# Optimization experiments

Hardware: AMD Instinct MI355X
Metric: run time of the kernel (lower is better)

Reference implementation:

```python
import jax, jax.numpy as jnp
import numpy as np

EPS = 1e-4

@jax.custom_vjp
def binarize(x):
    # BinaryConnectDeterministic: sign with sign(0)=+1
    return jnp.where(x >= 0, 1.0, -1.0).astype(x.dtype)

def _bin_fwd(x):
    return binarize(x), x

def _bin_bwd(x, g):
    # straight-through estimator, clipped to |x| <= 1
    return (g * (jnp.abs(x) <= 1).astype(g.dtype),)

binarize.defvjp(_bin_fwd, _bin_bwd)

def ap2(x):
    # approximate power-of-2: sign(x) * 2^round(log2|x|); grad is 0 a.e. (round/sign)
    a = jnp.maximum(jnp.abs(x), 1e-38)
    return jnp.sign(x) * jnp.exp2(jnp.round(jnp.log2(a)))

def shift_bn(x, gamma, beta, axes):
    # shift-based batch norm (BNN paper): var approximated via centered*AP2(centered),
    # inverse std and gamma replaced by their AP2 approximations. Training-mode batch stats.
    mean = jnp.mean(x, axis=axes, keepdims=True)
    c = x - mean
    var = jnp.mean(c * ap2(c), axis=axes, keepdims=True)
    xhat = c * ap2(1.0 / jnp.sqrt(var + EPS))
    shape = [1] * x.ndim
    shape[1] = x.shape[1]
    return ap2(gamma.reshape(shape)) * xhat + beta.reshape(shape)

def conv_bin(x, w, b):
    y = jax.lax.conv_general_dilated(x, binarize(w), (1, 1), [(1, 1), (1, 1)],
                                     dimension_numbers=('NCHW', 'OIHW', 'NCHW'))
    return y + b[None, :, None, None]

def maxpool3s2(x):
    return jax.lax.reduce_window(x, -jnp.inf, jax.lax.max,
                                 (1, 1, 3, 3), (1, 1, 2, 2), 'VALID')


def setup_inputs() -> dict:
    key = jax.random.key(0)
    ks = jax.random.split(key, 8)
    B, NU = 2048, 2048
    inp = {
        'x': jax.random.normal(ks[0], (B, 784), jnp.float32),
        'conv1_w': jax.random.normal(ks[1], (32, 1, 3, 3), jnp.float32) * 0.1,
        'conv1_b': jnp.zeros((32,), jnp.float32),
        'g1': jnp.ones((32,), jnp.float32), 'b1': jnp.zeros((32,), jnp.float32),
        'conv2_w': jax.random.normal(ks[2], (64, 32, 3, 3), jnp.float32) * 0.1,
        'conv2_b': jnp.zeros((64,), jnp.float32),
        'g2': jnp.ones((64,), jnp.float32), 'b2': jnp.zeros((64,), jnp.float32),
        'lin3_w': jax.random.normal(ks[3], (NU, 10816), jnp.float32) * 0.02,
        'lin3_b': jnp.zeros((NU,), jnp.float32),
        'g3': jnp.ones((NU,), jnp.float32), 'b3': jnp.zeros((NU,), jnp.float32),
        'lin4_w': jax.random.normal(ks[4], (10, NU), jnp.float32) * 0.02,
        'lin4_b': jnp.zeros((10,), jnp.float32),
    }
    return inp


def reference(x, conv1_w, conv1_b, g1, b1, conv2_w, conv2_b, g2, b2,
              lin3_w, lin3_b, g3, b3, lin4_w, lin4_b):
    h = x.reshape(-1, 1, 28, 28)
    h = jax.nn.relu(conv_bin(h, conv1_w, conv1_b))
    h = shift_bn(h, g1, b1, axes=(0, 2, 3))
    h = binarize(h)
    h = jax.nn.relu(conv_bin(h, conv2_w, conv2_b))
    h = maxpool3s2(h)                       # [B,64,13,13]
    h = shift_bn(h, g2, b2, axes=(0, 2, 3))
    h = binarize(h)
    h = h.reshape(h.shape[0], -1)           # [B,10816]
    h = jax.nn.relu(h @ binarize(lin3_w).T + lin3_b)
    h = shift_bn(h, g3, b3, axes=(0,))
    h = binarize(h)
    return h @ binarize(lin4_w).T + lin4_b  # [B,10] (no norm4/logsoftmax in forward)
```

## Files before the change

kernel.cpp:

```cpp
#include <hip/hip_runtime.h>

#define BB 2048
#define IMG 784
#define HWD 28
#define C1 32
#define C2 64
#define PP 169
#define PD 13
#define F3 10816
#define N3 2048
#define K4W 32
#define NOUT 10
#define CONV 27
#define PADW 30
#define OCCHUNK 8
#define IMGC 29
#define SCRP 740

typedef unsigned long long u64;
typedef int v4i __attribute__((ext_vector_type(4)));
typedef int v16i __attribute__((ext_vector_type(16)));

#define GLOAD16(gp, lp) __builtin_amdgcn_global_load_lds( \
    (__attribute__((address_space(1))) void*)(gp),        \
    (__attribute__((address_space(3))) void*)(lp), 16, 0, 0)

__device__ __forceinline__ float ap2mag(float c) {
    unsigned int a = __float_as_uint(c) & 0x7fffffffu;
    unsigned int e = (a >> 23) + ((a & 0x7fffffu) > 0x3504f3u);
    return __uint_as_float(e << 23);
}
__device__ __forceinline__ float ap2sgn(float g) {
    unsigned int u = __float_as_uint(g);
    unsigned int a = u & 0x7fffffffu;
    if (a == 0) return 0.f;
    unsigned int e = (a >> 23) + ((a & 0x7fffffu) > 0x3504f3u);
    return __uint_as_float((u & 0x80000000u) | (e << 23));
}

__global__ __launch_bounds__(256) void stage0(const float* __restrict__ x,
                                              const float* __restrict__ w1, const float* __restrict__ cb1,
                                              float* __restrict__ part1, float* __restrict__ w1b,
                                              const float* __restrict__ w2, char* __restrict__ w2i8,
                                              const float* __restrict__ w3, char* __restrict__ wp3i,
                                              const float* __restrict__ w4, u64* __restrict__ wp4) {
    __shared__ float xs[30 * PADW];
    __shared__ float red[4 * C1];
    int n = blockIdx.x, tid = threadIdx.x;
    int lane = tid & 63, wv = tid >> 6;
    {
        int idx = n * 256 + tid;
        int nthr = gridDim.x * 256;
        int total = (N3 * F3) / 4;
        for (int t = idx; t < total; t += nthr) {
            float4 wv4 = *(const float4*)(w3 + (size_t)t * 4);
            unsigned int w = (wv4.x >= 0.f ? 0x01u : 0xffu)
                           | (wv4.y >= 0.f ? 0x01u : 0xffu) << 8
                           | (wv4.z >= 0.f ? 0x01u : 0xffu) << 16
                           | (wv4.w >= 0.f ? 0x01u : 0xffu) << 24;
            *(unsigned int*)(wp3i + (size_t)t * 4) = w;
        }
    }
    if (n == 0) {
        for (int i = tid; i < C1 * 9; i += 256) w1b[i] = (w1[i] >= 0.f) ? 1.f : -1.f;
    } else if (n == 1) {
        for (int i = tid; i < 2 * 9 * 64 * 16; i += 256) {
            int hf = i / 9216;
            int r = i - hf * 9216;
            int t = r >> 10;
            int l = (r >> 4) & 63;
            int j = i & 15;
            int oc = hf * 32 + (l & 31);
            int ic = ((l >> 5) << 4) + j;
            w2i8[i] = (w2[oc * 288 + ic * 9 + t] >= 0.f) ? (char)1 : (char)(-1);
        }
    } else if (n == 2) {
        for (int w = wv; w < NOUT * K4W; w += 4) {
            int o = w / K4W, j = w % K4W;
            float wvl = w4[o * N3 + j * 64 + lane];
            u64 mask = __ballot(wvl >= 0.f);
            if (lane == 0) wp4[w] = mask;
        }
    }
    for (int i = tid; i < 30 * PADW; i += 256) {
        int r = i / PADW - 1, c = i % PADW - 1;
        float v = 0.f;
        if (r >= 0 && r < HWD && c >= 0 && c < HWD) v = x[n * IMG + r * HWD + c];
        xs[i] = v;
    }
    __syncthreads();
    bool act = tid < 196;
    int r = tid / 7, c0 = (tid % 7) * 4;
    float win[18];
#pragma unroll
    for (int k = 0; k < 18; k++) win[k] = 0.f;
    if (act) {
#pragma unroll
        for (int ry = 0; ry < 3; ry++)
#pragma unroll
            for (int cx = 0; cx < 6; cx++)
                win[ry * 6 + cx] = xs[(r + ry) * PADW + c0 + cx];
    }
#pragma unroll
    for (int ch = 0; ch < C1; ch++) {
        float a = 0.f;
        if (act) {
            float k0 = (w1[ch * 9 + 0] >= 0.f) ? 1.f : -1.f, k1 = (w1[ch * 9 + 1] >= 0.f) ? 1.f : -1.f;
            float k2 = (w1[ch * 9 + 2] >= 0.f) ? 1.f : -1.f, k3 = (w1[ch * 9 + 3] >= 0.f) ? 1.f : -1.f;
            float k4 = (w1[ch * 9 + 4] >= 0.f) ? 1.f : -1.f, k5 = (w1[ch * 9 + 5] >= 0.f) ? 1.f : -1.f;
            float k6 = (w1[ch * 9 + 6] >= 0.f) ? 1.f : -1.f, k7 = (w1[ch * 9 + 7] >= 0.f) ? 1.f : -1.f;
            float k8 = (w1[ch * 9 + 8] >= 0.f) ? 1.f : -1.f;
            float b = cb1[ch];
#pragma unroll
            for (int px = 0; px < 4; px++) {
                float s = win[px] * k0 + win[px + 1] * k1 + win[px + 2] * k2
                        + win[6 + px] * k3 + win[7 + px] * k4 + win[8 + px] * k5
                        + win[12 + px] * k6 + win[13 + px] * k7 + win[14 + px] * k8;
                a += fmaxf(s + b, 0.f);
            }
        }
        for (int off = 32; off; off >>= 1) a += __shfl_down(a, off);
        if (lane == 0) red[wv * C1 + ch] = a;
    }
    __syncthreads();
    if (tid < C1) part1[n * C1 + tid] = red[tid] + red[C1 + tid] + red[2 * C1 + tid] + red[3 * C1 + tid];
}

__global__ __launch_bounds__(256) void conv1_var(const float* __restrict__ x,
                            const float* __restrict__ w1b,
                            const float* __restrict__ cb1, const float* __restrict__ mean1,
                            float* __restrict__ part) {
    __shared__ float xs[30 * PADW];
    __shared__ float red[4 * C1];
    int n = blockIdx.x, tid = threadIdx.x;
    for (int i = tid; i < 30 * PADW; i += 256) {
        int r = i / PADW - 1, c = i % PADW - 1;
        float v = 0.f;
        if (r >= 0 && r < HWD && c >= 0 && c < HWD) v = x[n * IMG + r * HWD + c];
        xs[i] = v;
    }
    __syncthreads();
    bool act = tid < 196;
    int r = tid / 7, c0 = (tid % 7) * 4;
    float win[18];
#pragma unroll
    for (int k = 0; k < 18; k++) win[k] = 0.f;
    if (act) {
#pragma unroll
        for (int ry = 0; ry < 3; ry++)
#pragma unroll
            for (int cx = 0; cx < 6; cx++)
                win[ry * 6 + cx] = xs[(r + ry) * PADW + c0 + cx];
    }
    int lane = tid & 63, wv = tid >> 6;
#pragma unroll
    for (int ch = 0; ch < C1; ch++) {
        float a = 0.f;
        if (act) {
            float k0 = w1b[ch * 9 + 0], k1 = w1b[ch * 9 + 1], k2 = w1b[ch * 9 + 2];
            float k3 = w1b[ch * 9 + 3], k4 = w1b[ch * 9 + 4], k5 = w1b[ch * 9 + 5];
            float k6 = w1b[ch * 9 + 6], k7 = w1b[ch * 9 + 7], k8 = w1b[ch * 9 + 8];
            float b = cb1[ch], m = mean1[ch];
#pragma unroll
            for (int px = 0; px < 4; px++) {
                float s = win[px] * k0 + win[px + 1] * k1 + win[px + 2] * k2
                        + win[6 + px] * k3 + win[7 + px] * k4 + win[8 + px] * k5
                        + win[12 + px] * k6 + win[13 + px] * k7 + win[14 + px] * k8;
                float v = fmaxf(s + b, 0.f);
                float c = v - m;
                a += fabsf(c) * ap2mag(c);
            }
        }
        for (int off = 32; off; off >>= 1) a += __shfl_down(a, off);
        if (lane == 0) red[wv * C1 + ch] = a;
    }
    __syncthreads();
    if (tid < C1) part[n * C1 + tid] = red[tid] + red[C1 + tid] + red[2 * C1 + tid] + red[3 * C1 + tid];
}

__global__ __launch_bounds__(256) void conv1_pack(const float* __restrict__ x,
                           const float* __restrict__ w1b,
                           const float* __restrict__ cb1, const float* __restrict__ mean1,
                           const float* __restrict__ scale1, const float* __restrict__ beta1,
                           unsigned int* __restrict__ s1p) {
    __shared__ float xs[30 * PADW];
    int n = blockIdx.x, tid = threadIdx.x;
    for (int i = tid; i < 30 * PADW; i += 256) {
        int r = i / PADW - 1, c = i % PADW - 1;
        float v = 0.f;
        if (r >= 0 && r < HWD && c >= 0 && c < HWD) v = x[n * IMG + r * HWD + c];
        xs[i] = v;
    }
    __syncthreads();
    if (tid >= 196) return;
    int r = tid / 7, c0 = (tid % 7) * 4;
    float win[18];
#pragma unroll
    for (int ry = 0; ry < 3; ry++)
#pragma unroll
        for (int cx = 0; cx < 6; cx++)
            win[ry * 6 + cx] = xs[(r + ry) * PADW + c0 + cx];
    unsigned int bits0 = 0, bits1 = 0, bits2 = 0, bits3 = 0;
#pragma unroll
    for (int ch = 0; ch < C1; ch++) {
        float k0 = w1b[ch * 9 + 0], k1 = w1b[ch * 9 + 1], k2 = w1b[ch * 9 + 2];
        float k3 = w1b[ch * 9 + 3], k4 = w1b[ch * 9 + 4], k5 = w1b[ch * 9 + 5];
        float k6 = w1b[ch * 9 + 6], k7 = w1b[ch * 9 + 7], k8 = w1b[ch * 9 + 8];
        float b = cb1[ch], m = mean1[ch], sc = scale1[ch], bt = beta1[ch];
#pragma unroll
        for (int px = 0; px < 4; px++) {
            float s = win[px] * k0 + win[px + 1] * k1 + win[px + 2] * k2
                    + win[6 + px] * k3 + win[7 + px] * k4 + win[8 + px] * k5
                    + win[12 + px] * k6 + win[13 + px] * k7 + win[14 + px] * k8;
            float v = fmaxf(s + b, 0.f);
            float val = sc * (v - m) + bt;
            unsigned int bit = (val >= 0.f ? 1u : 0u) << ch;
            if (px == 0) bits0 |= bit;
            else if (px == 1) bits1 |= bit;
            else if (px == 2) bits2 |= bit;
            else bits3 |= bit;
        }
    }
    uint4 w4v = make_uint4(bits0, bits1, bits2, bits3);
    *reinterpret_cast<uint4*>(&s1p[n * IMG + r * HWD + c0]) = w4v;
}

__global__ __launch_bounds__(256) void conv2pool(const unsigned int* __restrict__ s1p,
                                                 const char* __restrict__ w2i8,
                                                 const float* __restrict__ cb2,
                                                 short* __restrict__ p2i,
                                                 float* __restrict__ part2) {
    __shared__ char img[IMGC * IMGC * 32];
    __shared__ short scr[32 * SCRP];
    __shared__ float psum[OCCHUNK * PP];
    __shared__ float pm[C2];
    int n = blockIdx.x, tid = threadIdx.x;
    int lane = tid & 63, wv = tid >> 6;
    for (int i = tid; i < IMGC * IMGC; i += 256) {
        int r = i / IMGC, c = i - r * IMGC;
        unsigned int w = 0u;
        if (r >= 1 && c >= 1) w = s1p[n * IMG + (r - 1) * HWD + (c - 1)];
        unsigned int d[8];
        if (r == 0 || c == 0) {
#pragma unroll
            for (int e = 0; e < 8; e++) d[e] = 0u;
        } else {
#pragma unroll
            for (int e = 0; e < 8; e++) {
                unsigned int nib = (w >> (4 * e)) & 0xFu;
                unsigned int t = (nib & 1u) | ((nib & 2u) << 7) | ((nib & 4u) << 14) | ((nib & 8u) << 21);
                d[e] = 0xFFFFFFFFu - t * 0xFEu;
            }
        }
        *(uint4*)&img[i * 32] = make_uint4(d[0], d[1], d[2], d[3]);
        *(uint4*)&img[i * 32 + 16] = make_uint4(d[4], d[5], d[6], d[7]);
    }
    __syncthreads();
    int hh = lane >> 5;
    int l31 = lane & 31;
    for (int hf = 0; hf < 2; hf++) {
        v4i bf[9];
#pragma unroll
        for (int t = 0; t < 9; t++)
            bf[t] = *(const v4i*)(w2i8 + (hf * 9 + t) * 1024 + lane * 16);
#pragma unroll
        for (int j = 0; j < 3; j++) {
            int mtA = wv + 8 * j, mtB = mtA + 4;
            int pA = mtA * 32 + l31; if (pA > 728) pA = 728;
            int pB = mtB * 32 + l31; if (pB > 728) pB = 728;
            int yA = pA / 27, xA = pA - yA * 27;
            int yB = pB / 27, xB = pB - yB * 27;
            int aA = (yA * IMGC + xA) * 32 + hh * 16;
            int aB = (yB * IMGC + xB) * 32 + hh * 16;
            v16i accA = {0,0,0,0,0,0,0,0,0,0,0,0,0,0,0,0};
            v16i accB = {0,0,0,0,0,0,0,0,0,0,0,0,0,0,0,0};
#pragma unroll
            for (int ky = 0; ky < 3; ky++)
#pragma unroll
                for (int kx = 0; kx < 3; kx++) {
                    v4i fA = *(const v4i*)&img[aA + (ky * IMGC + kx) * 32];
                    v4i fB = *(const v4i*)&img[aB + (ky * IMGC + kx) * 32];
                    accA = __builtin_amdgcn_mfma_i32_32x32x32_i8(fA, bf[ky * 3 + kx], accA, 0, 0, 0);
                    accB = __builtin_amdgcn_mfma_i32_32x32x32_i8(fB, bf[ky * 3 + kx], accB, 0, 0, 0);
                }
            short* sr = &scr[l31 * SCRP];
#pragma unroll
            for (int g = 0; g < 4; g++) {
                short4 sA;
                sA.x = (short)accA[4 * g + 0]; sA.y = (short)accA[4 * g + 1];
                sA.z = (short)accA[4 * g + 2]; sA.w = (short)accA[4 * g + 3];
                *(short4*)&sr[mtA * 32 + g * 8 + 4 * hh] = sA;
            }
            if (mtB < 23) {
#pragma unroll
                for (int g = 0; g < 4; g++) {
                    short4 sB;
                    sB.x = (short)accB[4 * g + 0]; sB.y = (short)accB[4 * g + 1];
                    sB.z = (short)accB[4 * g + 2]; sB.w = (short)accB[4 * g + 3];
                    *(short4*)&sr[mtB * 32 + g * 8 + 4 * hh] = sB;
                }
            }
        }
        __syncthreads();
        for (int base = 0; base < 32; base += OCCHUNK) {
            for (int q = tid; q < OCCHUNK * PP; q += 256) {
                int ol = q / PP, pix = q - ol * PP;
                int py = pix / PD, px = pix - py * PD;
                const short* rr = &scr[(base + ol) * SCRP + (2 * py) * CONV + 2 * px];
                int m0 = max(max((int)rr[0], (int)rr[1]), (int)rr[2]);
                int m1 = max(max((int)rr[CONV], (int)rr[CONV + 1]), (int)rr[CONV + 2]);
                int m2 = max(max((int)rr[2 * CONV], (int)rr[2 * CONV + 1]), (int)rr[2 * CONV + 2]);
                int val = max(max(m0, m1), m2);
                int oc = hf * 32 + base + ol;
                p2i[n * F3 + oc * PP + pix] = (short)val;
                psum[q] = fmaxf((float)val + cb2[oc], 0.f);
            }
            __syncthreads();
            for (int ol = wv; ol < OCCHUNK; ol += 4) {
                float a = 0.f;
                for (int pp = lane; pp < PP; pp += 64) a += psum[ol * PP + pp];
                for (int off = 32; off; off >>= 1) a += __shfl_down(a, off);
                if (lane == 0) pm[hf * 32 + base + ol] = a;
            }
            __syncthreads();
        }
    }
    if (tid < C2) part2[n * C2 + tid] = pm[tid];
}

__global__ __launch_bounds__(256) void p2_var(const short* __restrict__ p2i,
                         const float* __restrict__ cb2,
                         const float* __restrict__ mean2, float* __restrict__ part) {
    int n = blockIdx.x, tid = threadIdx.x, lane = tid & 63, wv = tid >> 6;
    const short* rowb = p2i + (size_t)n * F3;
    __shared__ float red[C2];
#pragma unroll
    for (int i = 0; i < 16; i++) {
        int ch = wv * 16 + i;
        const short* row = rowb + ch * PP;
        float b = cb2[ch];
        float m = mean2[ch];
        float a = 0.f;
        for (int p = lane; p < PP; p += 64) {
            float v = fmaxf((float)row[p] + b, 0.f);
            float c = v - m;
            a += fabsf(c) * ap2mag(c);
        }
        for (int off = 32; off; off >>= 1) a += __shfl_down(a, off);
        if (lane == 0) red[ch] = a;
    }
    __syncthreads();
    if (tid < C2) part[n * C2 + tid] = red[tid];
}

__global__ __launch_bounds__(256) void reduce_stats(const float* __restrict__ part, int nch, int nblk,
                             const float* __restrict__ g, float* __restrict__ outv,
                             int mode, double count) {
    int ch = blockIdx.x, tid = threadIdx.x;
    double a = 0.0;
    for (int i = tid; i < nblk; i += 256) a += (double)part[(size_t)i * nch + ch];
    __shared__ double red[4];
    for (int off = 32; off; off >>= 1) a += __shfl_down(a, off);
    int lane = tid & 63, wv = tid >> 6;
    if (lane == 0) red[wv] = a;
    __syncthreads();
    if (tid == 0) {
        double s = red[0] + red[1] + red[2] + red[3];
        if (mode == 0) {
            outv[ch] = (float)(s / count);
        } else {
            float var = (float)(s / count);
            float inv = 1.0f / sqrtf(var + 1e-4f);
            outv[ch] = ap2sgn(g[ch]) * ap2mag(inv);
        }
    }
}

__global__ __launch_bounds__(256) void p2_packi8(const short* __restrict__ p2i, const float* __restrict__ cb2,
                        const float* __restrict__ mean2, const float* __restrict__ scale2,
                        const float* __restrict__ beta2, char* __restrict__ hp3i) {
    int idx = blockIdx.x * 256 + threadIdx.x;
    int nthr = gridDim.x * 256;
    int total = (BB * F3) / 4;
    for (int t = idx; t < total; t += nthr) {
        int base = t * 4;
        int f0 = base % F3;
        unsigned int w = 0;
#pragma unroll
        for (int e = 0; e < 4; e++) {
            int f = f0 + e;
            int oc = f / PP;
            float v = fmaxf((float)p2i[base + e] + cb2[oc], 0.f);
            float val = scale2[oc] * (v - mean2[oc]) + beta2[oc];
            w |= (val >= 0.f ? 0x01u : 0xffu) << (8 * e);
        }
        *(unsigned int*)(hp3i + base) = w;
    }
}

__global__ __launch_bounds__(512) void lin3_mfma(const char* __restrict__ hp3i,
                                                 const char* __restrict__ wp3i,
                                                 const float* __restrict__ b3l,
                                                 float* __restrict__ h3,
                                                 float* __restrict__ h3T,
                                                 float* __restrict__ part3) {
    __shared__ v4i aL[3][1024];
    __shared__ v4i bL[3][1024];
    __shared__ float csr[8][32];
    int tid = threadIdx.x;
    int lane = tid & 63, wv = tid >> 6;
    int wr = wv >> 2, wc = wv & 3;
    int m0 = blockIdx.y * 128, n0 = blockIdx.x * 128;
    int loff = (lane & 15) * F3 + (lane >> 4) * 16;
    const char* gA = hp3i + (size_t)(m0 + wv * 16) * F3 + loff;
    const char* gB = wp3i + (size_t)(n0 + wv * 16) * F3 + loff;
    v4i acc[4][2];
#pragma unroll
    for (int i = 0; i < 4; i++)
#pragma unroll
        for (int j = 0; j < 2; j++) acc[i][j] = (v4i){0, 0, 0, 0};

    auto stage = [&](int c) {
        int b = c % 3;
        const char* pA = gA + (size_t)c * 128;
        const char* pB = gB + (size_t)c * 128;
        char* dA = (char*)&aL[b][0] + wv * 1024;
        char* dB = (char*)&bL[b][0] + wv * 1024;
        GLOAD16(pA,      dA);
        GLOAD16(pA + 64, dA + 8192);
        GLOAD16(pB,      dB);
        GLOAD16(pB + 64, dB + 8192);
    };
    auto compute = [&](int c, int nks) {
        int b = c % 3;
        for (int ks = 0; ks < nks; ++ks) {
            v4i af[4], bf[2];
#pragma unroll
            for (int i = 0; i < 4; i++) af[i] = aL[b][ks * 512 + (wr * 4 + i) * 64 + lane];
#pragma unroll
            for (int j = 0; j < 2; j++) bf[j] = bL[b][ks * 512 + (wc * 2 + j) * 64 + lane];
            __builtin_amdgcn_s_setprio(1);
#pragma unroll
            for (int i = 0; i < 4; i++)
#pragma unroll
                for (int j = 0; j < 2; j++)
                    acc[i][j] = __builtin_amdgcn_mfma_i32_16x16x64_i8(af[i], bf[j], acc[i][j], 0, 0, 0);
            __builtin_amdgcn_s_setprio(0);
        }
    };

    stage(0); stage(1);
    asm volatile("s_waitcnt vmcnt(4)" ::: "memory");
    __builtin_amdgcn_s_barrier();
    __builtin_amdgcn_sched_barrier(0);
    for (int c = 0; c < 83; ++c) {
        stage(c + 2);
        compute(c, 2);
        asm volatile("s_waitcnt vmcnt(4)" ::: "memory");
        __builtin_amdgcn_s_barrier();
        __builtin_amdgcn_sched_barrier(0);
    }
    compute(83, 2);
    asm volatile("s_waitcnt vmcnt(0)" ::: "memory");
    __builtin_amdgcn_s_barrier();
    __builtin_amdgcn_sched_barrier(0);
    compute(84, 1);

    int q = lane >> 4, m16 = lane & 15;
    float cs[2] = {0.f, 0.f};
#pragma unroll
    for (int j = 0; j < 2; j++) {
        int col = n0 + wc * 32 + j * 16 + m16;
        float bias = b3l[col];
#pragma unroll
        for (int i = 0; i < 4; i++) {
            int rowb = m0 + wr * 64 + i * 16 + q * 4;
            float4 t4;
#pragma unroll
            for (int rg = 0; rg < 4; rg++) {
                float v = fmaxf((float)acc[i][j][rg] + bias, 0.f);
                h3[(size_t)(rowb + rg) * N3 + col] = v;
                ((float*)&t4)[rg] = v;
                cs[j] += v;
            }
            *(float4*)&h3T[(size_t)col * BB + rowb] = t4;
        }
    }
#pragma unroll
    for (int j = 0; j < 2; j++) {
        cs[j] += __shfl_xor(cs[j], 16);
        cs[j] += __shfl_xor(cs[j], 32);
        if (lane < 16) csr[wv][j * 16 + m16] = cs[j];
    }
    __syncthreads();
    if (tid < 128) {
        int wcg = tid >> 5, cc = tid & 31;
        part3[(size_t)blockIdx.y * N3 + n0 + tid] = csr[wcg][cc] + csr[4 + wcg][cc];
    }
}

__global__ __launch_bounds__(256) void h3_finish(const float* __restrict__ h3T,
                                                 const float* __restrict__ part3,
                                                 const float* __restrict__ g3,
                                                 float* __restrict__ mean3, float* __restrict__ scale3) {
    int nn = blockIdx.x, tid = threadIdx.x;
    __shared__ float msh;
    __shared__ double redd[4];
    if (tid < 64) {
        float a = (tid < 16) ? part3[(size_t)tid * N3 + nn] : 0.f;
        for (int off = 8; off; off >>= 1) a += __shfl_down(a, off);
        if (tid == 0) { float m = a / (float)BB; mean3[nn] = m; msh = m; }
    }
    __syncthreads();
    float m = msh;
    float acc = 0.f;
#pragma unroll
    for (int q = 0; q < 8; q++) {
        float v = h3T[(size_t)nn * BB + q * 256 + tid];
        float c = v - m;
        acc += fabsf(c) * ap2mag(c);
    }
    double a = (double)acc;
    for (int off = 32; off; off >>= 1) a += __shfl_down(a, off);
    int lane = tid & 63, wv = tid >> 6;
    if (lane == 0) redd[wv] = a;
    __syncthreads();
    if (tid == 0) {
        float var = (float)((redd[0] + redd[1] + redd[2] + redd[3]) / (double)BB);
        float inv = 1.0f / sqrtf(var + 1e-4f);
        scale3[nn] = ap2sgn(g3[nn]) * ap2mag(inv);
    }
}

__global__ __launch_bounds__(256) void h4_out(const float* __restrict__ h3,
                                              const float* __restrict__ mean3, const float* __restrict__ scale3,
                                              const float* __restrict__ bt3,
                                              const u64* __restrict__ wp4, const float* __restrict__ b4,
                                              float* __restrict__ out) {
    __shared__ u64 hb[K4W];
    __shared__ u64 wsh[NOUT * 33];
    int m = blockIdx.x, tid = threadIdx.x, lane = tid & 63, wv = tid >> 6;
    for (int i = tid; i < NOUT * K4W; i += 256) wsh[(i / K4W) * 33 + (i % K4W)] = wp4[i];
#pragma unroll
    for (int q = 0; q < 8; q++) {
        int j = wv * 8 + q;
        int f = j * 64 + lane;
        float v = h3[(size_t)m * N3 + f];
        float val = scale3[f] * (v - mean3[f]) + bt3[f];
        u64 mask = __ballot(val >= 0.f);
        if (lane == 0) hb[j] = mask;
    }
    __syncthreads();
    if (tid < NOUT) {
        int c = 0;
#pragma unroll
        for (int k = 0; k < K4W; k++) c += (int)__popcll(hb[k] ^ wsh[tid * 33 + k]);
        out[m * NOUT + tid] = (float)(N3 - 2 * c) + b4[tid];
    }
}

extern "C" void kernel_launch(void* const* d_in, const int* in_sizes, int n_in,
                              void* d_out, int out_size, void* d_ws, size_t ws_size,
                              hipStream_t stream) {
    const float* x   = (const float*)d_in[0];
    const float* w1  = (const float*)d_in[1];
    const float* cb1 = (const float*)d_in[2];
    const float* g1  = (const float*)d_in[3];
    const float* bt1 = (const float*)d_in[4];
    const float* w2  = (const float*)d_in[5];
    const float* cb2 = (const float*)d_in[6];
    const float* g2  = (const float*)d_in[7];
    const float* bt2 = (const float*)d_in[8];
    const float* w3  = (const float*)d_in[9];
    const float* b3l = (const float*)d_in[10];
    const float* g3  = (const float*)d_in[11];
    const float* bt3 = (const float*)d_in[12];
    const float* w4  = (const float*)d_in[13];
    const float* b4l = (const float*)d_in[14];
    float* out = (float*)d_out;

    char* base = (char*)d_ws;
    size_t off = 0;
    auto carve = [&](size_t bytes) { char* p = base + off; off = (off + bytes + 255) & ~(size_t)255; return p; };
    char* bufA = carve((size_t)BB * C2 * PP * 2);
    char* bufB = carve((size_t)BB * F3);
    char* bufC = carve((size_t)N3 * F3);
    short* p2i         = (short*)bufA;
    float* h3          = (float*)bufA;
    float* h3T         = (float*)(bufA + (size_t)BB * N3 * 4);
    char* hp3i         = bufB;
    unsigned int* s1p  = (unsigned int*)bufB;
    char* wp3i         = bufC;
    u64* wp4           = (u64*)carve((size_t)NOUT * K4W * 8);
    char* w2i8         = (char*)carve((size_t)2 * 9 * 64 * 16);
    float* w1b         = (float*)carve((size_t)C1 * 9 * 4);
    float* part1       = (float*)carve((size_t)BB * C1 * 4);
    float* part2       = (float*)carve((size_t)BB * C2 * 4);
    float* part3       = (float*)carve((size_t)16 * N3 * 4);
    float* fstats      = (float*)carve((size_t)(32 + 32 + 64 + 64 + 2048 + 2048) * 4);
    float* mean1 = fstats;          float* scale1 = fstats + 32;
    float* mean2 = fstats + 64;     float* scale2 = fstats + 128;
    float* mean3 = fstats + 192;    float* scale3 = fstats + 2240;

    stage0<<<BB, 256, 0, stream>>>(x, w1, cb1, part1, w1b, w2, w2i8, w3, wp3i, w4, wp4);
    reduce_stats<<<C1, 256, 0, stream>>>(part1, C1, BB, g1, mean1, 0, (double)BB * IMG);
    conv1_var<<<BB, 256, 0, stream>>>(x, w1b, cb1, mean1, part1);
    reduce_stats<<<C1, 256, 0, stream>>>(part1, C1, BB, g1, scale1, 1, (double)BB * IMG);
    conv1_pack<<<BB, 256, 0, stream>>>(x, w1b, cb1, mean1, scale1, bt1, s1p);
    conv2pool<<<BB, 256, 0, stream>>>(s1p, w2i8, cb2, p2i, part2);
    reduce_stats<<<C2, 256, 0, stream>>>(part2, C2, BB, g2, mean2, 0, (double)BB * PP);
    p2_var<<<BB, 256, 0, stream>>>(p2i, cb2, mean2, part2);
    reduce_stats<<<C2, 256, 0, stream>>>(part2, C2, BB, g2, scale2, 1, (double)BB * PP);
    p2_packi8<<<2048, 256, 0, stream>>>(p2i, cb2, mean2, scale2, bt2, hp3i);
    lin3_mfma<<<dim3(16, 16), 512, 0, stream>>>(hp3i, wp3i, b3l, h3, h3T, part3);
    h3_finish<<<N3, 256, 0, stream>>>(h3T, part3, g3, mean3, scale3);
    h4_out<<<BB, 256, 0, stream>>>(h3, mean3, scale3, bt3, wp4, b4l, out);

    (void)in_sizes; (void)n_in; (void)out_size; (void)ws_size;
}
```

Baseline: 557.9 us.

## Split lin3 int8 GEMM along K into two partitions with separate reduction kernel

The lin3 int8 MFMA GEMM grid gains a split-K dimension of two, so 512 blocks run instead of 256 and more of the MI355X's compute units are occupied. Each half writes raw int32 accumulators to a new workspace buffer. A new lin3_fin kernel sums the two partials and performs the bias/ReLU/transposed store and column-sum epilogue. The pipeline also drops from triple-buffered LDS with fine-grained vmcnt waits to double buffering with __syncthreads, which shrinks LDS per block but may expose more load latency. It adds a 32 MB write and read of partials plus an extra launch.

```diff
diff --git a/kernel.cpp b/kernel.cpp
--- a/kernel.cpp
+++ b/kernel.cpp
@@ -400,20 +400,20 @@
 
 __global__ __launch_bounds__(512) void lin3_mfma(const char* __restrict__ hp3i,
                                                  const char* __restrict__ wp3i,
-                                                 const float* __restrict__ b3l,
-                                                 float* __restrict__ h3,
-                                                 float* __restrict__ h3T,
-                                                 float* __restrict__ part3) {
-    __shared__ v4i aL[3][1024];
-    __shared__ v4i bL[3][1024];
-    __shared__ float csr[8][32];
+                                                 int* __restrict__ cpart) {
+    __shared__ v4i aL[2][1024];
+    __shared__ v4i bL[2][1024];
     int tid = threadIdx.x;
     int lane = tid & 63, wv = tid >> 6;
     int wr = wv >> 2, wc = wv & 3;
     int m0 = blockIdx.y * 128, n0 = blockIdx.x * 128;
+    int kp = blockIdx.z;
+    int kbase = kp ? 5440 : 0;
+    int NC = kp ? 42 : 43;
+    int lastks = kp ? 2 : 1;
     int loff = (lane & 15) * F3 + (lane >> 4) * 16;
-    const char* gA = hp3i + (size_t)(m0 + wv * 16) * F3 + loff;
-    const char* gB = wp3i + (size_t)(n0 + wv * 16) * F3 + loff;
+    const char* gA = hp3i + (size_t)(m0 + wv * 16) * F3 + kbase + loff;
+    const char* gB = wp3i + (size_t)(n0 + wv * 16) * F3 + kbase + loff;
     v4i acc[4][2];
 #pragma unroll
     for (int i = 0; i < 4; i++)
@@ -421,7 +421,7 @@
         for (int j = 0; j < 2; j++) acc[i][j] = (v4i){0, 0, 0, 0};
 
     auto stage = [&](int c) {
-        int b = c % 3;
+        int b = c & 1;
         const char* pA = gA + (size_t)c * 128;
         const char* pB = gB + (size_t)c * 128;
         char* dA = (char*)&aL[b][0] + wv * 1024;
@@ -432,7 +432,7 @@
         GLOAD16(pB + 64, dB + 8192);
     };
     auto compute = [&](int c, int nks) {
-        int b = c % 3;
+        int b = c & 1;
         for (int ks = 0; ks < nks; ++ks) {
             v4i af[4], bf[2];
 #pragma unroll
@@ -449,23 +449,43 @@
         }
     };
 
-    stage(0); stage(1);
-    asm volatile("s_waitcnt vmcnt(4)" ::: "memory");
-    __builtin_amdgcn_s_barrier();
-    __builtin_amdgcn_sched_barrier(0);
-    for (int c = 0; c < 83; ++c) {
-        stage(c + 2);
-        compute(c, 2);
-        asm volatile("s_waitcnt vmcnt(4)" ::: "memory");
-        __builtin_amdgcn_s_barrier();
-        __builtin_amdgcn_sched_barrier(0);
-    }
-    compute(83, 2);
-    asm volatile("s_waitcnt vmcnt(0)" ::: "memory");
-    __builtin_amdgcn_s_barrier();
-    __builtin_amdgcn_sched_barrier(0);
-    compute(84, 1);
-
+    stage(0);
+    __syncthreads();
+    for (int c = 0; c < NC; ++c) {
+        if (c < NC - 1) stage(c + 1);
+        compute(c, (c == NC - 1) ? lastks : 2);
+        __syncthreads();
+    }
+    int* cp = cpart + ((size_t)kp * 256 + (size_t)blockIdx.y * 16 + blockIdx.x) * 16384;
+#pragma unroll
+    for (int i = 0; i < 4; i++)
+#pragma unroll
+        for (int j = 0; j < 2; j++)
+            *(v4i*)&cp[(((i * 2 + j) * 512) + tid) * 4] = acc[i][j];
+}
+
+__global__ __launch_bounds__(512) void lin3_fin(const int* __restrict__ cpart,
+                                                const float* __restrict__ b3l,
+                                                float* __restrict__ h3,
+                                                float* __restrict__ h3T,
+                                                float* __restrict__ part3) {
+    __shared__ float csr[8][32];
+    int tid = threadIdx.x;
+    int lane = tid & 63, wv = tid >> 6;
+    int wr = wv >> 2, wc = wv & 3;
+    int m0 = blockIdx.y * 128, n0 = blockIdx.x * 128;
+    const int* c0 = cpart + ((size_t)blockIdx.y * 16 + blockIdx.x) * 16384;
+    const int* c1 = c0 + (size_t)256 * 16384;
+    v4i acc[4][2];
+#pragma unroll
+    for (int i = 0; i < 4; i++)
+#pragma unroll
+        for (int j = 0; j < 2; j++) {
+            int s = (((i * 2 + j) * 512) + tid) * 4;
+            v4i a = *(const v4i*)&c0[s];
+            v4i b = *(const v4i*)&c1[s];
+            acc[i][j] = a + b;
+        }
     int q = lane >> 4, m16 = lane & 15;
     float cs[2] = {0.f, 0.f};
 #pragma unroll
@@ -591,6 +611,7 @@
     char* hp3i         = bufB;
     unsigned int* s1p  = (unsigned int*)bufB;
     char* wp3i         = bufC;
+    int* cpart         = (int*)carve((size_t)2 * BB * N3 * 4);
     u64* wp4           = (u64*)carve((size_t)NOUT * K4W * 8);
     char* w2i8         = (char*)carve((size_t)2 * 9 * 64 * 16);
     float* w1b         = (float*)carve((size_t)C1 * 9 * 4);
@@ -612,7 +633,8 @@
     p2_var<<<BB, 256, 0, stream>>>(p2i, cb2, mean2, part2);
     reduce_stats<<<C2, 256, 0, stream>>>(part2, C2, BB, g2, scale2, 1, (double)BB * PP);
     p2_packi8<<<2048, 256, 0, stream>>>(p2i, cb2, mean2, scale2, bt2, hp3i);
-    lin3_mfma<<<dim3(16, 16), 512, 0, stream>>>(hp3i, wp3i, b3l, h3, h3T, part3);
+    lin3_mfma<<<dim3(16, 16, 2), 512, 0, stream>>>(hp3i, wp3i, cpart);
+    lin3_fin<<<dim3(16, 16), 512, 0, stream>>>(cpart, b3l, h3, h3T, part3);
     h3_finish<<<N3, 256, 0, stream>>>(h3T, part3, g3, mean3, scale3);
     h4_out<<<BB, 256, 0, stream>>>(h3, mean3, scale3, bt3, wp4, b4l, out);
 
```

After: 523.0 us. 6.2% less time.
